# Performance work log

Measured on AMD Instinct MI355X. Metric: run time of the kernel, lower is better.

Reference implementation:

```python
import jax, jax.numpy as jnp
import numpy as np

BINS = 128  # histogram_bins from init


def setup_inputs() -> dict:
    key = jax.random.key(0)
    k1, k2, k3 = jax.random.split(key, 3)
    B, F, OUT = 4096, 16384, 64
    x = jax.random.normal(k1, (B, F), dtype=jnp.float32)
    # nn.Linear(2*bins+1, out) params
    fan_in = 2 * BINS + 1
    lim = 1.0 / np.sqrt(fan_in)
    W = jax.random.uniform(k2, (OUT, fan_in), dtype=jnp.float32, minval=-lim, maxval=lim)
    b = jax.random.uniform(k3, (OUT,), dtype=jnp.float32, minval=-lim, maxval=lim)
    return {"x": x, "W": W, "b": b}


def _histogram_features(x):
    # x: [B, F] (already flattened). Per-row torch.histc with min/max = row min/max.
    B, F = x.shape
    mn = x.min(axis=1, keepdims=True)                      # [B, 1]
    mx = x.max(axis=1, keepdims=True)                      # [B, 1]
    width = mx - mn
    # bin index: floor((v - min) * bins / (max - min)), clamped so v == max lands in last bin
    idx = jnp.floor((x - mn) * (BINS / jnp.where(width == 0, 1.0, width))).astype(jnp.int32)
    idx = jnp.clip(idx, 0, BINS - 1)                       # [B, F]
    # single fused scatter across the whole batch
    flat_idx = (jnp.arange(B, dtype=jnp.int32)[:, None] * BINS + idx).reshape(-1)
    counts = jax.ops.segment_sum(
        jnp.ones((B * F,), dtype=x.dtype), flat_idx, num_segments=B * BINS
    ).reshape(B, BINS)
    counts = counts / counts.sum(axis=1, keepdims=True)    # density=True
    # boundaries = linspace(min, max, bins+1) per row
    t = jnp.linspace(0.0, 1.0, BINS + 1, dtype=x.dtype)    # [bins+1]
    boundaries = mn + t[None, :] * width                   # [B, bins+1]
    return jnp.concatenate([counts, boundaries], axis=1)   # [B, 2*bins+1]


def reference(x, W, b):
    B = x.shape[0]
    feats = _histogram_features(x.reshape(B, -1))
    feats = jax.lax.stop_gradient(feats)  # torch wraps histogram in no_grad
    return feats @ W.T + b
```

## Files before the change

kernel.cpp:

```cpp
#include <hip/hip_runtime.h>


#define BINS   128
#define FEAT   16384
#define NOUT   64
#define TPB    1024
#define NWAVE  (TPB / 64)
#define PER_T  (FEAT / TPB)
#define NFEATS (2 * BINS + 1)

__global__ __launch_bounds__(TPB) void hist_row_kernel(
    const float* __restrict__ x,
    const float* __restrict__ W,
    const float* __restrict__ b,
    float* __restrict__ out)
{
    __shared__ unsigned int s_hist[NWAVE][BINS];
    __shared__ float s_red[2 * NWAVE];
    __shared__ float s_counts[BINS];
    __shared__ float s_mm[2];

    const int row  = blockIdx.x;
    const int tid  = threadIdx.x;
    const int lane = tid & 63;
    const int wave = tid >> 6;

    #pragma unroll
    for (int i = tid; i < NWAVE * BINS; i += TPB)
        ((unsigned int*)s_hist)[i] = 0u;

    const float4* xr = (const float4*)(x + (size_t)row * FEAT);
    float4 v[PER_T / 4];
    float mn = INFINITY, mx = -INFINITY;
    #pragma unroll
    for (int c = 0; c < PER_T / 4; ++c) {
        v[c] = xr[c * TPB + tid];
        mn = fminf(mn, fminf(fminf(v[c].x, v[c].y), fminf(v[c].z, v[c].w)));
        mx = fmaxf(mx, fmaxf(fmaxf(v[c].x, v[c].y), fmaxf(v[c].z, v[c].w)));
    }

    #pragma unroll
    for (int off = 32; off > 0; off >>= 1) {
        mn = fminf(mn, __shfl_down(mn, off));
        mx = fmaxf(mx, __shfl_down(mx, off));
    }
    if (lane == 0) { s_red[wave] = mn; s_red[NWAVE + wave] = mx; }
    __syncthreads();
    if (tid == 0) {
        float m0 = s_red[0], m1 = s_red[NWAVE];
        #pragma unroll
        for (int i = 1; i < NWAVE; ++i) {
            m0 = fminf(m0, s_red[i]);
            m1 = fmaxf(m1, s_red[NWAVE + i]);
        }
        s_mm[0] = m0; s_mm[1] = m1;
    }
    __syncthreads();
    const float rmn   = s_mm[0];
    const float rmx   = s_mm[1];
    const float width = rmx - rmn;
    const float scale = (float)BINS / (width == 0.0f ? 1.0f : width);

    unsigned int* hw = s_hist[wave];
    #pragma unroll
    for (int c = 0; c < PER_T / 4; ++c) {
        const float vv[4] = {v[c].x, v[c].y, v[c].z, v[c].w};
        #pragma unroll
        for (int k = 0; k < 4; ++k) {
            int idx = (int)floorf((vv[k] - rmn) * scale);
            idx = idx < 0 ? 0 : (idx > BINS - 1 ? BINS - 1 : idx);
            atomicAdd(&hw[idx], 1u);
        }
    }
    __syncthreads();

    if (tid < BINS) {
        unsigned int s = 0;
        #pragma unroll
        for (int wv = 0; wv < NWAVE; ++wv) s += s_hist[wv][tid];
        s_counts[tid] = (float)s * (1.0f / (float)FEAT);
    }
    __syncthreads();

    const int o   = tid >> 4;
    const int sub = tid & 15;
    float acc = 0.0f;
    const float* Wo = W + o * NFEATS;
    for (int j = sub; j < NFEATS; j += 16) {
        const float f = (j < BINS)
            ? s_counts[j]
            : rmn + (float)(j - BINS) * (1.0f / (float)BINS) * width;
        acc += f * Wo[j];
    }
    #pragma unroll
    for (int off = 8; off > 0; off >>= 1)
        acc += __shfl_down(acc, off, 16);
    if (sub == 0)
        out[(size_t)row * NOUT + o] = acc + b[o];
}

extern "C" void kernel_launch(void* const* d_in, const int* in_sizes, int n_in,
                              void* d_out, int out_size, void* d_ws, size_t ws_size,
                              hipStream_t stream) {
    const float* x = (const float*)d_in[0];
    const float* W = (const float*)d_in[1];
    const float* b = (const float*)d_in[2];
    float* out = (float*)d_out;

    hist_row_kernel<<<4096, TPB, 0, stream>>>(x, W, b, out);
}
```

Measured before the change: 368.6 us.

## Use smaller blocks, re-read row for binning, lane-spread padded histogram copies

Block size drops from 1024 to 256 threads with a launch-bounds occupancy hint, and the per-thread register array holding the whole row is removed. The row is now read twice from global memory (once for min/max, once for binning), relying on cache hits for the second pass. Per-wave histograms are replaced by 16 lane-indexed copies with a stride of 129 to spread LDS atomic conflicts across banks. The cost is doubled global load traffic for each row and a longer serial loop per thread.

```diff
diff --git a/kernel.cpp b/kernel.cpp
--- a/kernel.cpp
+++ b/kernel.cpp
@@ -1,21 +1,23 @@
 #include <hip/hip_runtime.h>
 
 
-#define BINS   128
-#define FEAT   16384
-#define NOUT   64
-#define TPB    1024
-#define NWAVE  (TPB / 64)
-#define PER_T  (FEAT / TPB)
-#define NFEATS (2 * BINS + 1)
+#define BINS    128
+#define FEAT    16384
+#define NOUT    64
+#define TPB     256
+#define NWAVE   (TPB / 64)
+#define NCPY    16
+#define HSTRIDE 129
+#define NFEATS  (2 * BINS + 1)
+#define PER_T4  (FEAT / 4 / TPB)
 
-__global__ __launch_bounds__(TPB) void hist_row_kernel(
+__global__ __launch_bounds__(TPB, 8) void hist_row_kernel(
     const float* __restrict__ x,
     const float* __restrict__ W,
     const float* __restrict__ b,
     float* __restrict__ out)
 {
-    __shared__ unsigned int s_hist[NWAVE][BINS];
+    __shared__ unsigned int s_hist[NCPY * HSTRIDE];
     __shared__ float s_red[2 * NWAVE];
     __shared__ float s_counts[BINS];
     __shared__ float s_mm[2];
@@ -25,51 +27,47 @@
     const int lane = tid & 63;
     const int wave = tid >> 6;
 
-    #pragma unroll
-    for (int i = tid; i < NWAVE * BINS; i += TPB)
-        ((unsigned int*)s_hist)[i] = 0u;
+    for (int i = tid; i < NCPY * HSTRIDE; i += TPB) s_hist[i] = 0u;
 
     const float4* xr = (const float4*)(x + (size_t)row * FEAT);
-    float4 v[PER_T / 4];
     float mn = INFINITY, mx = -INFINITY;
+    #pragma unroll 4
+    for (int i = 0; i < PER_T4; ++i) {
+        float4 t = xr[i * TPB + tid];
+        mn = fminf(mn, fminf(fminf(t.x, t.y), fminf(t.z, t.w)));
+        mx = fmaxf(mx, fmaxf(fmaxf(t.x, t.y), fmaxf(t.z, t.w)));
+    }
     #pragma unroll
-    for (int c = 0; c < PER_T / 4; ++c) {
-        v[c] = xr[c * TPB + tid];
-        mn = fminf(mn, fminf(fminf(v[c].x, v[c].y), fminf(v[c].z, v[c].w)));
-        mx = fmaxf(mx, fmaxf(fmaxf(v[c].x, v[c].y), fmaxf(v[c].z, v[c].w)));
-    }
-
-    #pragma unroll
-    for (int off = 32; off > 0; off >>= 1) {
+    for (int off = 32; off; off >>= 1) {
         mn = fminf(mn, __shfl_down(mn, off));
         mx = fmaxf(mx, __shfl_down(mx, off));
     }
     if (lane == 0) { s_red[wave] = mn; s_red[NWAVE + wave] = mx; }
     __syncthreads();
     if (tid == 0) {
-        float m0 = s_red[0], m1 = s_red[NWAVE];
+        float a = s_red[0], c = s_red[NWAVE];
         #pragma unroll
         for (int i = 1; i < NWAVE; ++i) {
-            m0 = fminf(m0, s_red[i]);
-            m1 = fmaxf(m1, s_red[NWAVE + i]);
+            a = fminf(a, s_red[i]);
+            c = fmaxf(c, s_red[NWAVE + i]);
         }
-        s_mm[0] = m0; s_mm[1] = m1;
+        s_mm[0] = a; s_mm[1] = c;
     }
     __syncthreads();
     const float rmn   = s_mm[0];
-    const float rmx   = s_mm[1];
-    const float width = rmx - rmn;
+    const float width = s_mm[1] - rmn;
     const float scale = (float)BINS / (width == 0.0f ? 1.0f : width);
 
-    unsigned int* hw = s_hist[wave];
-    #pragma unroll
-    for (int c = 0; c < PER_T / 4; ++c) {
-        const float vv[4] = {v[c].x, v[c].y, v[c].z, v[c].w};
+    unsigned int* hc = s_hist + (tid & (NCPY - 1)) * HSTRIDE;
+    #pragma unroll 2
+    for (int i = 0; i < PER_T4; ++i) {
+        float4 t = xr[i * TPB + tid];
+        const float vv[4] = {t.x, t.y, t.z, t.w};
         #pragma unroll
         for (int k = 0; k < 4; ++k) {
             int idx = (int)floorf((vv[k] - rmn) * scale);
             idx = idx < 0 ? 0 : (idx > BINS - 1 ? BINS - 1 : idx);
-            atomicAdd(&hw[idx], 1u);
+            atomicAdd(&hc[idx], 1u);
         }
     }
     __syncthreads();
@@ -77,26 +75,24 @@
     if (tid < BINS) {
         unsigned int s = 0;
         #pragma unroll
-        for (int wv = 0; wv < NWAVE; ++wv) s += s_hist[wv][tid];
+        for (int c = 0; c < NCPY; ++c) s += s_hist[c * HSTRIDE + tid];
         s_counts[tid] = (float)s * (1.0f / (float)FEAT);
     }
     __syncthreads();
 
-    const int o   = tid >> 4;
-    const int sub = tid & 15;
+    const int o   = tid >> 2;
+    const int sub = tid & 3;
     float acc = 0.0f;
     const float* Wo = W + o * NFEATS;
-    for (int j = sub; j < NFEATS; j += 16) {
+    for (int j = sub; j < NFEATS; j += 4) {
         const float f = (j < BINS)
             ? s_counts[j]
             : rmn + (float)(j - BINS) * (1.0f / (float)BINS) * width;
         acc += f * Wo[j];
     }
-    #pragma unroll
-    for (int off = 8; off > 0; off >>= 1)
-        acc += __shfl_down(acc, off, 16);
-    if (sub == 0)
-        out[(size_t)row * NOUT + o] = acc + b[o];
+    acc += __shfl_down(acc, 2, 4);
+    acc += __shfl_down(acc, 1, 4);
+    if (sub == 0) out[(size_t)row * NOUT + o] = acc + b[o];
 }
 
 extern "C" void kernel_launch(void* const* d_in, const int* in_sizes, int n_in,
```

Result: slower. 408.0 us (+10.7%).
